# Kernel tuning notes

Hardware: AMD Instinct MI355X
Metric: run time of the kernel (lower is better)

The kernel has to match this reference:

```python
import jax, jax.numpy as jnp
import numpy as np

NUM_CLASSES = 8
NUM_MAPS = 4
FEAT_C = 2048  # ResNet-50 layer4 channels
HW = 14        # spatial size (448/32)


def setup_inputs() -> dict:
    key = jax.random.key(0)
    k1, k2, k3, k4, k5 = jax.random.split(key, 5)
    B = 64
    x = jax.random.normal(k1, (B, FEAT_C, HW, HW), dtype=jnp.float32)
    down_w = jax.random.normal(k2, (NUM_CLASSES * NUM_MAPS, FEAT_C), dtype=jnp.float32) * 0.02
    down_b = jax.random.normal(k3, (NUM_CLASSES * NUM_MAPS,), dtype=jnp.float32) * 0.02
    fc_w = jax.random.normal(k4, (NUM_CLASSES, 2 * FEAT_C), dtype=jnp.float32) * 0.02
    fc_b = jax.random.normal(k5, (NUM_CLASSES,), dtype=jnp.float32) * 0.02
    return {"x": x, "down_w": down_w, "down_b": down_b, "fc_w": fc_w, "fc_b": fc_b}


def reference(x, down_w, down_b, fc_w, fc_b):
    B = x.shape[0]
    x_ori = x  # [B, 2048, 14, 14] (ResNet features output)
    # downconv: 1x1 conv 2048 -> num_classes*num_maps
    xc = jnp.einsum('bchw,oc->bohw', x_ori, down_w) + down_b[None, :, None, None]  # [B,32,14,14]
    # GMP over full 14x14 window -> [B, 32]
    gmp = jnp.max(xc, axis=(2, 3))
    # spatial_pooling = ClassWisePool(num_maps): mean over groups of num_maps channels
    scores = gmp.reshape(B, NUM_CLASSES, NUM_MAPS).mean(axis=2)  # [B, 8]
    x_out = jax.nn.log_softmax(scores, axis=1)  # first output
    # class-wise pool on the full conv map: [B,32,14,14] -> [B,8,14,14]
    xcp = xc.reshape(B, NUM_CLASSES, NUM_MAPS, HW, HW).mean(axis=2)
    # modulate each class map by its (log-softmax) score
    xcp = xcp * x_out[:, :, None, None]
    # spatial_pooling2 = ClassWisePool(num_classes): mean over 8 class channels -> [B,1,14,14]
    sal = xcp.mean(axis=1, keepdims=True)
    prod = sal * x_ori  # [B,2048,14,14] via broadcast (fused, no copies)
    cat = jnp.concatenate([x_ori, prod], axis=1)  # [B,4096,14,14]
    # GAP 14x14 -> [B,4096]
    gap = cat.mean(axis=(2, 3))
    logits2 = gap @ fc_w.T + fc_b  # [B,8]
    x_conv_out = jax.nn.log_softmax(logits2, axis=1)
    return (x_out, x_conv_out)
```

## Files before the change

kernel.cpp:

```cpp
#include <hip/hip_runtime.h>

#define NCH 2048
#define HW 196
#define NB 64
#define NOUT 48
#define NCHUNK 8
#define CPC (NCH / NCHUNK)
#define KS_PER_BLK (CPC / 32)
#define KGTOT (NCH / 32)
#define NT 13
#define MT 3
#define TILE_F (32 * HW)
#define TILE_V4 (TILE_F / 4)
#define SLAB (NT * NOUT * 16)
#define SLAB4 (SLAB / 4)

typedef __attribute__((ext_vector_type(8))) short bf16x8;
typedef __attribute__((ext_vector_type(4))) float f32x4;
typedef __attribute__((ext_vector_type(4))) int i32x4;

__device__ __forceinline__ short f2bf(float f) {
    unsigned int u = __float_as_uint(f);
    u = u + 0x7fffu + ((u >> 16) & 1u);
    return (short)(u >> 16);
}

__global__ void build_afrag(const float* __restrict__ down_w,
                            const float* __restrict__ fc_w,
                            bf16x8* __restrict__ afrag) {
    int t = blockIdx.x * 256 + threadIdx.x;
    if (t >= KGTOT * MT * 64) return;
    int lane = t & 63;
    int frag = t >> 6;
    int mt = frag % MT;
    int kg = frag / MT;
    int o = mt * 16 + (lane & 15);
    int cbase = kg * 32 + (lane >> 4) * 8;
    bf16x8 v;
#pragma unroll
    for (int j = 0; j < 8; ++j) {
        int c = cbase + j;
        float w;
        if (o < 32)      w = down_w[o * NCH + c];
        else if (o < 40) w = fc_w[(o - 32) * (2 * NCH) + NCH + c];
        else             w = fc_w[(o - 40) * (2 * NCH) + c];
        v[j] = f2bf(w);
    }
    afrag[frag * 64 + lane] = v;
}

__global__ __launch_bounds__(256) void conv_mfma(const float* __restrict__ x,
                                                 const bf16x8* __restrict__ afrag,
                                                 float* __restrict__ part) {
    __shared__ float ldsx[2][TILE_F];
    const int chunk = blockIdx.x;
    const int b = blockIdx.y;
    const int tid = threadIdx.x;
    const int wave = tid >> 6;
    const int lane = tid & 63;
    const int nsub = lane & 15;
    const int kq = lane >> 4;

    f32x4 acc[4][MT];
#pragma unroll
    for (int i = 0; i < 4; ++i)
#pragma unroll
        for (int m = 0; m < MT; ++m)
            acc[i][m] = (f32x4){0.f, 0.f, 0.f, 0.f};

    int pidx[4];
#pragma unroll
    for (int i = 0; i < 4; ++i) {
        int p = (wave + 4 * i) * 16 + nsub;
        pidx[i] = (p < HW) ? p : (HW - 1);
    }

    const float* xtile0 = x + ((size_t)b * NCH + (size_t)chunk * CPC) * HW;

    auto stage = [&](int ks, int bb) {
        const float* g = xtile0 + (size_t)ks * TILE_F;
#pragma unroll
        for (int r = 0; r < 7; ++r) {
            int q = r * 256 + tid;
            if (q < TILE_V4) {
                __builtin_amdgcn_global_load_lds(
                    (const __attribute__((address_space(1))) unsigned int*)(g + (size_t)q * 4),
                    (__attribute__((address_space(3))) unsigned int*)(&ldsx[bb][(r * 256 + wave * 64) * 4]),
                    16, 0, 0);
            }
        }
    };

    stage(0, 0);

    for (int ks = 0; ks < KS_PER_BLK; ++ks) {
        __syncthreads();
        if (ks + 1 < KS_PER_BLK) stage(ks + 1, (ks + 1) & 1);

        const int kg = chunk * KS_PER_BLK + ks;
        bf16x8 a0 = afrag[(kg * MT + 0) * 64 + lane];
        bf16x8 a1 = afrag[(kg * MT + 1) * 64 + lane];
        bf16x8 a2 = afrag[(kg * MT + 2) * 64 + lane];

        const float* base = &ldsx[ks & 1][kq * 8 * HW];
#pragma unroll
        for (int i = 0; i < 4; ++i) {
            const float* bp = base + pidx[i];
            unsigned int u[8];
#pragma unroll
            for (int j = 0; j < 8; ++j)
                u[j] = __float_as_uint(bp[j * HW]) + 0x8000u;
            i32x4 bi;
            bi[0] = (int)__builtin_amdgcn_perm(u[1], u[0], 0x07060302u);
            bi[1] = (int)__builtin_amdgcn_perm(u[3], u[2], 0x07060302u);
            bi[2] = (int)__builtin_amdgcn_perm(u[5], u[4], 0x07060302u);
            bi[3] = (int)__builtin_amdgcn_perm(u[7], u[6], 0x07060302u);
            bf16x8 bv = __builtin_bit_cast(bf16x8, bi);
            acc[i][0] = __builtin_amdgcn_mfma_f32_16x16x32_bf16(a0, bv, acc[i][0], 0, 0, 0);
            acc[i][1] = __builtin_amdgcn_mfma_f32_16x16x32_bf16(a1, bv, acc[i][1], 0, 0, 0);
            acc[i][2] = __builtin_amdgcn_mfma_f32_16x16x32_bf16(a2, bv, acc[i][2], 0, 0, 0);
        }
    }

    float* pb = part + (size_t)(b * NCHUNK + chunk) * SLAB;
#pragma unroll
    for (int i = 0; i < 4; ++i) {
        int nt = wave + 4 * i;
        if (nt < NT) {
            float* d = pb + nt * (NOUT * 16) + kq * 64 + nsub;
#pragma unroll
            for (int m = 0; m < MT; ++m)
#pragma unroll
                for (int r = 0; r < 4; ++r)
                    d[m * 256 + r * 16] = acc[i][m][r];
        }
    }
}

__global__ __launch_bounds__(256) void finish(const float* __restrict__ part,
                                              const float* __restrict__ down_b,
                                              const float* __restrict__ fc_b,
                                              float* __restrict__ out) {
    const int b = blockIdx.x;
    const int tid = threadIdx.x;
    __shared__ float Ts[NOUT * HW];
    __shared__ float gmpS[32];
    __shared__ float scoreS[8];
    __shared__ float xoS[8];
    __shared__ float salS[HW];
    __shared__ float logitS[8];

    {
        const float4* base = (const float4*)(part + (size_t)b * NCHUNK * SLAB);
        for (int i4 = tid; i4 < SLAB4; i4 += 256) {
            float4 s = base[i4];
#pragma unroll
            for (int ch = 1; ch < NCHUNK; ++ch) {
                float4 v = base[(size_t)ch * SLAB4 + i4];
                s.x += v.x; s.y += v.y; s.z += v.z; s.w += v.w;
            }
            int nt = i4 / 192;
            int rem = i4 - nt * 192;
            int o = rem >> 2, ns4 = rem & 3;
            int p = nt * 16 + ns4 * 4;
            float vv[4] = {s.x, s.y, s.z, s.w};
#pragma unroll
            for (int q = 0; q < 4; ++q)
                if (p + q < HW) Ts[o * HW + p + q] = vv[q];
        }
    }
    __syncthreads();

    if (tid < 32) {
        float m = -1e30f;
        for (int p = 0; p < HW; ++p) m = fmaxf(m, Ts[tid * HW + p]);
        gmpS[tid] = m + down_b[tid];
    }
    __syncthreads();

    if (tid < 8)
        scoreS[tid] = 0.25f * (gmpS[4 * tid] + gmpS[4 * tid + 1] +
                               gmpS[4 * tid + 2] + gmpS[4 * tid + 3]);
    __syncthreads();

    if (tid < 8) {
        float m = -1e30f;
        for (int k = 0; k < 8; ++k) m = fmaxf(m, scoreS[k]);
        float se = 0.f;
        for (int k = 0; k < 8; ++k) se += expf(scoreS[k] - m);
        float xo = scoreS[tid] - m - logf(se);
        xoS[tid] = xo;
        out[b * 8 + tid] = xo;
    }
    __syncthreads();

    if (tid < HW) {
        float s = 0.f;
#pragma unroll
        for (int k = 0; k < 8; ++k) {
            float bs = down_b[4 * k] + down_b[4 * k + 1] +
                       down_b[4 * k + 2] + down_b[4 * k + 3];
            float rs = Ts[(4 * k) * HW + tid] + Ts[(4 * k + 1) * HW + tid] +
                       Ts[(4 * k + 2) * HW + tid] + Ts[(4 * k + 3) * HW + tid] + bs;
            s += xoS[k] * rs;
        }
        salS[tid] = s * (1.f / 32.f);
    }
    __syncthreads();

    if (tid < 8) {
        float t1 = 0.f, t2 = 0.f;
        for (int p = 0; p < HW; ++p) {
            t1 += Ts[(40 + tid) * HW + p];
            t2 += salS[p] * Ts[(32 + tid) * HW + p];
        }
        logitS[tid] = (t1 + t2) * (1.f / 196.f) + fc_b[tid];
    }
    __syncthreads();

    if (tid < 8) {
        float m = -1e30f;
        for (int k = 0; k < 8; ++k) m = fmaxf(m, logitS[k]);
        float se = 0.f;
        for (int k = 0; k < 8; ++k) se += expf(logitS[k] - m);
        out[NB * 8 + b * 8 + tid] = logitS[tid] - m - logf(se);
    }
}

extern "C" void kernel_launch(void* const* d_in, const int* in_sizes, int n_in,
                              void* d_out, int out_size, void* d_ws, size_t ws_size,
                              hipStream_t stream) {
    const float* x      = (const float*)d_in[0];
    const float* down_w = (const float*)d_in[1];
    const float* down_b = (const float*)d_in[2];
    const float* fc_w   = (const float*)d_in[3];
    const float* fc_b   = (const float*)d_in[4];
    float* out = (float*)d_out;

    bf16x8* afrag = (bf16x8*)d_ws;
    float* part = (float*)((char*)d_ws + (size_t)KGTOT * MT * 64 * 16);

    build_afrag<<<(KGTOT * MT * 64 + 255) / 256, 256, 0, stream>>>(down_w, fc_w, afrag);
    conv_mfma<<<dim3(NCHUNK, NB), 256, 0, stream>>>(x, afrag, part);
    finish<<<NB, 256, 0, stream>>>(part, down_b, fc_b, out);
}
```

Measured before the change: 183.9 us.

## Fuse finish into conv kernel via per-batch last-block atomic counter

Merges the separate finish kernel into the conv kernel. Each block stores its partials with atomic stores and bumps a per-batch counter, and the last-arriving block for that batch does the reduction and epilogue, reusing the LDS tile through a union. This removes one kernel launch and the gap between kernels. The max and logit loops now use all 256 threads in parallel reductions instead of 8 or 32 threads. The cost is serialized epilogue work on the last block and slower scalar atomic loads in place of the float4 loads.

```diff
diff --git a/kernel.cpp b/kernel.cpp
--- a/kernel.cpp
+++ b/kernel.cpp
@@ -13,7 +13,7 @@
 #define TILE_F (32 * HW)
 #define TILE_V4 (TILE_F / 4)
 #define SLAB (NT * NOUT * 16)
-#define SLAB4 (SLAB / 4)
+#define MAGICROW (NOUT * 16)
 
 typedef __attribute__((ext_vector_type(8))) short bf16x8;
 typedef __attribute__((ext_vector_type(4))) float f32x4;
@@ -27,8 +27,10 @@
 
 __global__ void build_afrag(const float* __restrict__ down_w,
                             const float* __restrict__ fc_w,
-                            bf16x8* __restrict__ afrag) {
+                            bf16x8* __restrict__ afrag,
+                            unsigned int* __restrict__ cnt) {
     int t = blockIdx.x * 256 + threadIdx.x;
+    if (blockIdx.x == 0 && threadIdx.x < NB) cnt[threadIdx.x] = 0;
     if (t >= KGTOT * MT * 64) return;
     int lane = t & 63;
     int frag = t >> 6;
@@ -49,10 +51,29 @@
     afrag[frag * 64 + lane] = v;
 }
 
-__global__ __launch_bounds__(256) void conv_mfma(const float* __restrict__ x,
-                                                 const bf16x8* __restrict__ afrag,
-                                                 float* __restrict__ part) {
-    __shared__ float ldsx[2][TILE_F];
+struct FinSM {
+    float Ts[NOUT * HW];
+    float red[256];
+    float gmp[32];
+    float score[8];
+    float xo[8];
+    float sal[HW];
+    float logit[8];
+};
+
+__global__ __launch_bounds__(256) void conv_fin(const float* __restrict__ x,
+                                                const bf16x8* __restrict__ afrag,
+                                                const float* __restrict__ down_b,
+                                                const float* __restrict__ fc_b,
+                                                float* __restrict__ part,
+                                                unsigned int* __restrict__ cnt,
+                                                float* __restrict__ out) {
+    __shared__ union {
+        float ldsx[2][TILE_F];
+        FinSM fin;
+    } sm;
+    __shared__ int lastS;
+
     const int chunk = blockIdx.x;
     const int b = blockIdx.y;
     const int tid = threadIdx.x;
@@ -85,7 +106,7 @@
             if (q < TILE_V4) {
                 __builtin_amdgcn_global_load_lds(
                     (const __attribute__((address_space(1))) unsigned int*)(g + (size_t)q * 4),
-                    (__attribute__((address_space(3))) unsigned int*)(&ldsx[bb][(r * 256 + wave * 64) * 4]),
+                    (__attribute__((address_space(3))) unsigned int*)(&sm.ldsx[bb][(r * 256 + wave * 64) * 4]),
                     16, 0, 0);
             }
         }
@@ -102,7 +123,7 @@
         bf16x8 a1 = afrag[(kg * MT + 1) * 64 + lane];
         bf16x8 a2 = afrag[(kg * MT + 2) * 64 + lane];
 
-        const float* base = &ldsx[ks & 1][kq * 8 * HW];
+        const float* base = &sm.ldsx[ks & 1][kq * 8 * HW];
 #pragma unroll
         for (int i = 0; i < 4; ++i) {
             const float* bp = base + pidx[i];
@@ -127,69 +148,72 @@
     for (int i = 0; i < 4; ++i) {
         int nt = wave + 4 * i;
         if (nt < NT) {
-            float* d = pb + nt * (NOUT * 16) + kq * 64 + nsub;
+            float* d = pb + nt * MAGICROW + kq * 64 + nsub;
 #pragma unroll
             for (int m = 0; m < MT; ++m)
 #pragma unroll
                 for (int r = 0; r < 4; ++r)
-                    d[m * 256 + r * 16] = acc[i][m][r];
-        }
-    }
-}
-
-__global__ __launch_bounds__(256) void finish(const float* __restrict__ part,
-                                              const float* __restrict__ down_b,
-                                              const float* __restrict__ fc_b,
-                                              float* __restrict__ out) {
-    const int b = blockIdx.x;
-    const int tid = threadIdx.x;
-    __shared__ float Ts[NOUT * HW];
-    __shared__ float gmpS[32];
-    __shared__ float scoreS[8];
-    __shared__ float xoS[8];
-    __shared__ float salS[HW];
-    __shared__ float logitS[8];
+                    __hip_atomic_store(&d[m * 256 + r * 16], acc[i][m][r],
+                                       __ATOMIC_RELAXED, __HIP_MEMORY_SCOPE_AGENT);
+        }
+    }
+
+    __syncthreads();
+    if (tid == 0) {
+        unsigned int old = __hip_atomic_fetch_add(&cnt[b], 1u,
+                                                  __ATOMIC_RELAXED, __HIP_MEMORY_SCOPE_AGENT);
+        int last = (old == NCHUNK - 1);
+        if (last)
+            (void)__hip_atomic_load(&cnt[b], __ATOMIC_ACQUIRE, __HIP_MEMORY_SCOPE_AGENT);
+        lastS = last;
+    }
+    __syncthreads();
+    if (!lastS) return;
 
     {
-        const float4* base = (const float4*)(part + (size_t)b * NCHUNK * SLAB);
-        for (int i4 = tid; i4 < SLAB4; i4 += 256) {
-            float4 s = base[i4];
-#pragma unroll
-            for (int ch = 1; ch < NCHUNK; ++ch) {
-                float4 v = base[(size_t)ch * SLAB4 + i4];
-                s.x += v.x; s.y += v.y; s.z += v.z; s.w += v.w;
-            }
-            int nt = i4 / 192;
-            int rem = i4 - nt * 192;
-            int o = rem >> 2, ns4 = rem & 3;
-            int p = nt * 16 + ns4 * 4;
-            float vv[4] = {s.x, s.y, s.z, s.w};
-#pragma unroll
-            for (int q = 0; q < 4; ++q)
-                if (p + q < HW) Ts[o * HW + p + q] = vv[q];
-        }
-    }
-    __syncthreads();
-
+        float* basep = part + (size_t)b * NCHUNK * SLAB;
+        for (int idx = tid; idx < SLAB; idx += 256) {
+            float s = 0.f;
+#pragma unroll
+            for (int ch = 0; ch < NCHUNK; ++ch)
+                s += __hip_atomic_load(&basep[(size_t)ch * SLAB + idx],
+                                       __ATOMIC_RELAXED, __HIP_MEMORY_SCOPE_AGENT);
+            int nt = idx / MAGICROW;
+            int rem = idx - nt * MAGICROW;
+            int o = rem >> 4, ns = rem & 15;
+            int p = nt * 16 + ns;
+            if (p < HW) sm.fin.Ts[o * HW + p] = s;
+        }
+    }
+    __syncthreads();
+
+    {
+        int o = tid >> 3, s8 = tid & 7;
+        float m = -1e30f;
+        for (int p = s8; p < HW; p += 8) m = fmaxf(m, sm.fin.Ts[o * HW + p]);
+        sm.fin.red[tid] = m;
+    }
+    __syncthreads();
     if (tid < 32) {
-        float m = -1e30f;
-        for (int p = 0; p < HW; ++p) m = fmaxf(m, Ts[tid * HW + p]);
-        gmpS[tid] = m + down_b[tid];
+        float m = sm.fin.red[tid * 8];
+#pragma unroll
+        for (int j = 1; j < 8; ++j) m = fmaxf(m, sm.fin.red[tid * 8 + j]);
+        sm.fin.gmp[tid] = m + down_b[tid];
     }
     __syncthreads();
 
     if (tid < 8)
-        scoreS[tid] = 0.25f * (gmpS[4 * tid] + gmpS[4 * tid + 1] +
-                               gmpS[4 * tid + 2] + gmpS[4 * tid + 3]);
+        sm.fin.score[tid] = 0.25f * (sm.fin.gmp[4 * tid] + sm.fin.gmp[4 * tid + 1] +
+                                     sm.fin.gmp[4 * tid + 2] + sm.fin.gmp[4 * tid + 3]);
     __syncthreads();
 
     if (tid < 8) {
         float m = -1e30f;
-        for (int k = 0; k < 8; ++k) m = fmaxf(m, scoreS[k]);
+        for (int k = 0; k < 8; ++k) m = fmaxf(m, sm.fin.score[k]);
         float se = 0.f;
-        for (int k = 0; k < 8; ++k) se += expf(scoreS[k] - m);
-        float xo = scoreS[tid] - m - logf(se);
-        xoS[tid] = xo;
+        for (int k = 0; k < 8; ++k) se += expf(sm.fin.score[k] - m);
+        float xo = sm.fin.score[tid] - m - logf(se);
+        sm.fin.xo[tid] = xo;
         out[b * 8 + tid] = xo;
     }
     __syncthreads();
@@ -200,30 +224,36 @@
         for (int k = 0; k < 8; ++k) {
             float bs = down_b[4 * k] + down_b[4 * k + 1] +
                        down_b[4 * k + 2] + down_b[4 * k + 3];
-            float rs = Ts[(4 * k) * HW + tid] + Ts[(4 * k + 1) * HW + tid] +
-                       Ts[(4 * k + 2) * HW + tid] + Ts[(4 * k + 3) * HW + tid] + bs;
-            s += xoS[k] * rs;
-        }
-        salS[tid] = s * (1.f / 32.f);
-    }
-    __syncthreads();
-
+            float rs = sm.fin.Ts[(4 * k) * HW + tid] + sm.fin.Ts[(4 * k + 1) * HW + tid] +
+                       sm.fin.Ts[(4 * k + 2) * HW + tid] + sm.fin.Ts[(4 * k + 3) * HW + tid] + bs;
+            s += sm.fin.xo[k] * rs;
+        }
+        sm.fin.sal[tid] = s * (1.f / 32.f);
+    }
+    __syncthreads();
+
+    {
+        int c = tid >> 5, s32 = tid & 31;
+        float t = 0.f;
+        for (int p = s32; p < HW; p += 32)
+            t += sm.fin.Ts[(40 + c) * HW + p] + sm.fin.sal[p] * sm.fin.Ts[(32 + c) * HW + p];
+        sm.fin.red[tid] = t;
+    }
+    __syncthreads();
     if (tid < 8) {
-        float t1 = 0.f, t2 = 0.f;
-        for (int p = 0; p < HW; ++p) {
-            t1 += Ts[(40 + tid) * HW + p];
-            t2 += salS[p] * Ts[(32 + tid) * HW + p];
-        }
-        logitS[tid] = (t1 + t2) * (1.f / 196.f) + fc_b[tid];
+        float t = 0.f;
+#pragma unroll
+        for (int j = 0; j < 32; ++j) t += sm.fin.red[tid * 32 + j];
+        sm.fin.logit[tid] = t * (1.f / 196.f) + fc_b[tid];
     }
     __syncthreads();
 
     if (tid < 8) {
         float m = -1e30f;
-        for (int k = 0; k < 8; ++k) m = fmaxf(m, logitS[k]);
+        for (int k = 0; k < 8; ++k) m = fmaxf(m, sm.fin.logit[k]);
         float se = 0.f;
-        for (int k = 0; k < 8; ++k) se += expf(logitS[k] - m);
-        out[NB * 8 + b * 8 + tid] = logitS[tid] - m - logf(se);
+        for (int k = 0; k < 8; ++k) se += expf(sm.fin.logit[k] - m);
+        out[NB * 8 + b * 8 + tid] = sm.fin.logit[tid] - m - logf(se);
     }
 }
 
@@ -239,8 +269,8 @@
 
     bf16x8* afrag = (bf16x8*)d_ws;
     float* part = (float*)((char*)d_ws + (size_t)KGTOT * MT * 64 * 16);
-
-    build_afrag<<<(KGTOT * MT * 64 + 255) / 256, 256, 0, stream>>>(down_w, fc_w, afrag);
-    conv_mfma<<<dim3(NCHUNK, NB), 256, 0, stream>>>(x, afrag, part);
-    finish<<<NB, 256, 0, stream>>>(part, down_b, fc_b, out);
-}
+    unsigned int* cnt = (unsigned int*)((char*)part + (size_t)NB * NCHUNK * SLAB * 4);
+
+    build_afrag<<<(KGTOT * MT * 64 + 255) / 256, 256, 0, stream>>>(down_w, fc_w, afrag, cnt);
+    conv_fin<<<dim3(NCHUNK, NB), 256, 0, stream>>>(x, afrag, down_b, fc_b, part, cnt, out);
+}
```

Result: no change. 185.4 us (+0.8%).
